# Performance work log

Hardware: AMD Instinct MI355X
Metric: run time of the kernel (lower is better)

The kernel has to match this reference:

```python
import jax, jax.numpy as jnp
import numpy as np

DN = ('NCHW', 'OIHW', 'NCHW')

def conv(x, w, b, stride=1, pad=1):
    y = jax.lax.conv_general_dilated(x, w, (stride, stride), [(pad, pad), (pad, pad)], dimension_numbers=DN)
    return y + b[None, :, None, None]

def conv_t(x, w, b):
    # torch ConvTranspose2d(k=4, s=2, p=1): implemented as lhs-dilated conv, pad = k-1-p = 2
    y = jax.lax.conv_general_dilated(x, w, (1, 1), [(2, 2), (2, 2)], lhs_dilation=(2, 2), dimension_numbers=DN)
    return y + b[None, :, None, None]

def residual_stack(x, rw3, rb3, rw1, rb1):
    # canonical VQ-VAE residual block: x + conv1x1(relu(conv3x3(relu(x)))), then final relu
    n = rw3.shape[0]
    for i in range(n):
        h = conv(jax.nn.relu(x), rw3[i], rb3[i], 1, 1)
        h = conv(jax.nn.relu(h), rw1[i], rb1[i], 1, 0)
        x = x + h
    return jax.nn.relu(x)

def vq(x, codebook, beta):
    # x: [N, D, H, W] -> [N, H, W, D]
    x = jnp.transpose(x, (0, 2, 3, 1))
    shp = x.shape
    xf = x.reshape(-1, shp[-1])                               # [T, D]
    d = (jnp.sum(xf * xf, 1, keepdims=True)
         + jnp.sum(codebook * codebook, 1)
         - 2.0 * xf @ codebook.T)                             # [T, K]
    idx = jnp.argmin(d, axis=1)                               # [T]
    enc = jax.nn.one_hot(idx, codebook.shape[0], dtype=x.dtype)
    q = jnp.take(codebook, idx, axis=0).reshape(shp)
    loss_e = jnp.mean((jax.lax.stop_gradient(q) - x) ** 2)
    loss_q = jnp.mean((q - jax.lax.stop_gradient(x)) ** 2)
    loss = loss_q + beta * loss_e
    q_st = x + jax.lax.stop_gradient(q - x)
    p = jnp.mean(enc, axis=0)
    perplexity = jnp.exp(-jnp.sum(p * jnp.log(p + 1e-10)))
    return loss, jnp.transpose(q_st, (0, 3, 1, 2)), perplexity, enc

def setup_inputs() -> dict:
    key = jax.random.key(0)
    ks = jax.random.split(key, 24)
    C_img, C, RH, NR, K, D = 3, 128, 32, 2, 512, 64
    def g(k, shape, fan_in):
        return jax.random.normal(k, shape, jnp.float32) * (1.0 / np.sqrt(fan_in))
    inp = {
        'x': jax.random.normal(ks[0], (16, C_img, 256, 256), jnp.float32),
        'enc_w1': g(ks[1], (C // 2, C_img, 4, 4), C_img * 16), 'enc_b1': jnp.zeros((C // 2,)),
        'enc_w2': g(ks[2], (C, C // 2, 4, 4), C // 2 * 16), 'enc_b2': jnp.zeros((C,)),
        'enc_w3': g(ks[3], (C, C, 3, 3), C * 9), 'enc_b3': jnp.zeros((C,)),
        'enc_rw3': g(ks[4], (NR, RH, C, 3, 3), C * 9), 'enc_rb3': jnp.zeros((NR, RH)),
        'enc_rw1': g(ks[5], (NR, C, RH, 1, 1), RH), 'enc_rb1': jnp.zeros((NR, C)),
        'pre_w': g(ks[6], (D, C, 1, 1), C), 'pre_b': jnp.zeros((D,)),
        'codebook': jax.random.uniform(ks[7], (K, D), jnp.float32, -1.0 / K, 1.0 / K),
        'dec_w1': g(ks[8], (C, D, 3, 3), D * 9), 'dec_b1': jnp.zeros((C,)),
        'dec_rw3': g(ks[9], (NR, RH, C, 3, 3), C * 9), 'dec_rb3': jnp.zeros((NR, RH)),
        'dec_rw1': g(ks[10], (NR, C, RH, 1, 1), RH), 'dec_rb1': jnp.zeros((NR, C)),
        'dec_dw1': g(ks[11], (C // 2, C, 4, 4), C * 16), 'dec_db1': jnp.zeros((C // 2,)),
        'dec_dw2': g(ks[12], (C_img, C // 2, 4, 4), C // 2 * 16), 'dec_db2': jnp.zeros((C_img,)),
    }
    return inp

def reference(x, enc_w1, enc_b1, enc_w2, enc_b2, enc_w3, enc_b3, enc_rw3, enc_rb3, enc_rw1, enc_rb1,
              pre_w, pre_b, codebook, dec_w1, dec_b1, dec_rw3, dec_rb3, dec_rw1, dec_rb1,
              dec_dw1, dec_db1, dec_dw2, dec_db2):
    beta = 0.25
    # encoder
    h = jax.nn.relu(conv(x, enc_w1, enc_b1, 2, 1))
    h = jax.nn.relu(conv(h, enc_w2, enc_b2, 2, 1))
    h = conv(h, enc_w3, enc_b3, 1, 1)
    h = residual_stack(h, enc_rw3, enc_rb3, enc_rw1, enc_rb1)
    # pre-VQ 1x1 conv
    z = conv(h, pre_w, pre_b, 1, 0)
    # vector quantization
    loss, q, perplexity, _ = vq(z, codebook, beta)
    # decoder
    d = conv(q, dec_w1, dec_b1, 1, 1)
    d = residual_stack(d, dec_rw3, dec_rb3, dec_rw1, dec_rb1)
    d = jax.nn.relu(conv_t(d, dec_dw1, dec_db1))
    x_recon = conv_t(d, dec_dw2, dec_db2)
    return loss, x_recon, perplexity
```

## Files before the change

kernel.cpp:

```cpp
#include <hip/hip_runtime.h>

typedef __attribute__((ext_vector_type(8)))  short bf16x8;
typedef __attribute__((ext_vector_type(16))) float f32x16;
typedef unsigned long long u64t;

__device__ __forceinline__ int swzu(int u)
{
    return u ^ (((u >> 3) & 1) | (((u >> 4) & 1) << 1));
}

__device__ __forceinline__ void fsplit(float v, unsigned short& h, unsigned short& l)
{
    union { float f; unsigned u; } a; a.f = v;
    unsigned uh = a.u + 0x7fffu + ((a.u >> 16) & 1u);
    h = (unsigned short)(uh >> 16);
    union { float f; unsigned u; } hb; hb.u = (unsigned)h << 16;
    float r = v - hb.f;
    union { float f; unsigned u; } b; b.f = r;
    unsigned ul = b.u + 0x7fffu + ((b.u >> 16) & 1u);
    l = (unsigned short)(ul >> 16);
}

__device__ __forceinline__ float bf2f(unsigned short u)
{
    union { float f; unsigned v; } a; a.v = (unsigned)u << 16; return a.f;
}

__global__ void pack_w(const float* __restrict__ w, unsigned short* __restrict__ hi,
                       unsigned short* __restrict__ lo, int Cout, int Cin, int KK,
                       int CoP, int CiP)
{
    int i = blockIdx.x * 256 + threadIdx.x;
    int tot = KK * CoP * CiP;
    if (i >= tot) return;
    int t  = i / (CoP * CiP);
    int r  = i - t * (CoP * CiP);
    int co = r / CiP;
    int ci = r - co * CiP;
    float v = (co < Cout && ci < Cin) ? w[((size_t)co * Cin + ci) * KK + t] : 0.f;
    unsigned short h, l;
    fsplit(v, h, l);
    hi[i] = h; lo[i] = l;
}

__global__ void cb_norm(const float* __restrict__ cb, float* __restrict__ cn)
{
    int i = blockIdx.x * 256 + threadIdx.x;
    if (i >= 512) return;
    float s = 0.f;
    for (int d = 0; d < 64; d++) s = fmaf(cb[i*64+d], cb[i*64+d], s);
    cn[i] = s;
}

__global__ __launch_bounds__(256) void pack_x(const float* __restrict__ x,
    unsigned short* __restrict__ PH)
{
    int idx = blockIdx.x * 256 + threadIdx.x;
    int n = idx >> 16, pix = idx & 65535;
    unsigned short h[8], l[8];
#pragma unroll
    for (int c = 0; c < 8; c++) h[c] = 0;
#pragma unroll
    for (int c = 0; c < 3; c++) {
        float v = x[((size_t)(n * 3 + c) << 16) + pix];
        fsplit(v, h[c], l[c]);
    }
    uint4 hv;
    hv.x = h[0] | ((unsigned)h[1] << 16); hv.y = h[2] | ((unsigned)h[3] << 16);
    hv.z = h[4] | ((unsigned)h[5] << 16); hv.w = h[6] | ((unsigned)h[7] << 16);
    uint4 z4 = make_uint4(0, 0, 0, 0);
    size_t b0 = (((size_t)(n * 2) << 16) + pix) * 8;
    size_t b1 = (((size_t)(n * 2 + 1) << 16) + pix) * 8;
    *(uint4*)(PH + b0) = hv;
    *(uint4*)(PH + b1) = z4;
}

template<int K,int S,int P,int CIP,int COUT,int HIN,int WIN,int HOUT,int WOUT,
         int TR,int TC,int WM,int WN,int PX2,int CO2,int CC,int CO_PAD,
         bool PACK,bool PRELU,bool PLO,bool WF32,bool ROUT,bool RES>
__global__ __launch_bounds__(256) void conv_mfma(
    const unsigned short* __restrict__ inH,
    const unsigned short* __restrict__ wpH,
    const float* __restrict__ bias, const float* __restrict__ res,
    float* __restrict__ outF, unsigned short* __restrict__ outPH,
    unsigned short* __restrict__ outPL)
{
    constexpr int IHT = (TR - 1) * S + K;
    constexpr int IW  = (TC - 1) * S + K;
    constexpr int PS  = IHT * IW;
    constexpr int PLN = CC * 2;
    constexpr int UN  = PS * PLN;
    constexpr int KK  = K * K;
    constexpr int NCH = CIP / (CC * 16);
    constexpr int CG  = CIP / 8;
    constexpr int CGO = (COUT + 7) / 8;
    constexpr int XB  = WOUT / TC;
    constexpr int REGU = (UN + 255) / 256;
    constexpr int NST = CC * KK;

    __shared__ uint4 lbH[UN];

    const int tid = threadIdx.x;
    const int bx  = blockIdx.x;
    const int r0  = (bx / XB) * TR;
    const int c0  = (bx % XB) * TC;
    const int co0 = blockIdx.y * (WM * CO2 * 32);
    const int n   = blockIdx.z;

    const int l  = tid & 63, wv = tid >> 6;
    const int wm = wv / WN, wn = wv % WN;
    const int ln = l & 31, kg = l >> 5;

    int pb[PX2], gyv[PX2], gxv[PX2];
#pragma unroll
    for (int p2 = 0; p2 < PX2; p2++) {
        int q = wn * (PX2 * 32) + p2 * 32 + ln;
        int lr = q / TC, lc = q % TC;
        pb[p2] = (lr * S) * IW + lc * S;
        gyv[p2] = r0 + lr; gxv[p2] = c0 + lc;
    }

    const int iy0 = r0 * S - P, ix0 = c0 * S - P;
    const size_t inb = (size_t)n * CG * HIN * WIN;

    f32x16 acc[PX2][CO2];
#pragma unroll
    for (int p2 = 0; p2 < PX2; p2++)
#pragma unroll
        for (int g = 0; g < CO2; g++) acc[p2][g] = (f32x16){};

    auto unit_load = [&](int u, int cgb, uint4& hv){
        int kgu = u / PS, pos = u - kgu * PS;
        int py = pos / IW, px = pos - py * IW;
        int gy = iy0 + py, gx = ix0 + px;
        bool ok = ((unsigned)gy < (unsigned)HIN) && ((unsigned)gx < (unsigned)WIN);
        hv = make_uint4(0,0,0,0);
        if (ok) {
            size_t a = (inb + ((size_t)(cgb + kgu) * HIN + gy) * WIN + gx) * 8;
            hv = *(const uint4*)(inH + a);
        }
    };

    auto stage_direct = [&](int kc){
        for (int idx = tid; idx < UN; idx += 256) {
            uint4 hv;
            unit_load(idx, kc * PLN, hv);
            lbH[swzu(idx)] = hv;
        }
    };

    uint4 rvH[REGU];
    auto load_regs = [&](int kc){
#pragma unroll
        for (int rr = 0; rr < REGU; rr++) {
            int idx = tid + rr * 256;
            uint4 hv = make_uint4(0,0,0,0);
            if (idx < UN) unit_load(idx, kc * PLN, hv);
            rvH[rr] = hv;
        }
    };
    auto write_regs = [&](){
#pragma unroll
        for (int rr = 0; rr < REGU; rr++) {
            int idx = tid + rr * 256;
            if (idx < UN) lbH[swzu(idx)] = rvH[rr];
        }
    };

    auto compute = [&](int kc){
        bf16x8 aC[CO2], aN[CO2], bC[PX2], bN[PX2];
        auto loadA = [&](int step, bf16x8* a){
            const int ks = step / KK, t = step - ks * KK;
#pragma unroll
            for (int g = 0; g < CO2; g++) {
                const int coA = co0 + (wm * CO2 + g) * 32 + ln;
                const size_t wo = ((size_t)t * CO_PAD + coA) * CIP
                                + kc * (CC * 16) + ks * 16 + kg * 8;
                a[g] = *(const bf16x8*)(wpH + wo);
            }
        };
        auto loadB = [&](int step, bf16x8* b){
            const int ks = step / KK, t = step - ks * KK;
            const int ky = t / K, kx = t - ky * K;
#pragma unroll
            for (int p2 = 0; p2 < PX2; p2++) {
                const int u = (ks * 2 + kg) * PS + pb[p2] + ky * IW + kx;
                b[p2] = *(const bf16x8*)&lbH[swzu(u)];
            }
        };
        loadA(0, aC); loadB(0, bC);
#pragma unroll
        for (int step = 0; step < NST; step++) {
            if (step + 1 < NST) { loadA(step + 1, aN); loadB(step + 1, bN); }
#pragma unroll
            for (int p2 = 0; p2 < PX2; p2++)
#pragma unroll
                for (int g = 0; g < CO2; g++)
                    acc[p2][g] = __builtin_amdgcn_mfma_f32_32x32x16_bf16(
                        aC[g], bC[p2], acc[p2][g], 0, 0, 0);
            if (step + 1 < NST) {
#pragma unroll
                for (int g = 0; g < CO2; g++) aC[g] = aN[g];
#pragma unroll
                for (int p2 = 0; p2 < PX2; p2++) bC[p2] = bN[p2];
            }
        }
    };

    stage_direct(0);
    __syncthreads();
    for (int kc = 0; kc < NCH; kc++) {
        const bool more = (kc + 1 < NCH);
        if (more) load_regs(kc + 1);
        compute(kc);
        if (more) {
            __syncthreads();
            write_regs();
            __syncthreads();
        }
    }

    const size_t HWo = (size_t)HOUT * WOUT;
#pragma unroll
    for (int p2 = 0; p2 < PX2; p2++) {
        const int gy = gyv[p2], gx = gxv[p2];
#pragma unroll
        for (int g = 0; g < CO2; g++) {
            const int co32 = co0 + (wm * CO2 + g) * 32;
#pragma unroll
            for (int rq = 0; rq < 4; rq++) {
                const int cb4 = co32 + 8 * rq + 4 * kg;
                float v[4];
#pragma unroll
                for (int i = 0; i < 4; i++) {
                    const int r = rq * 4 + i;
                    const int co = cb4 + i;
                    float bv = (co < COUT) ? bias[co] : 0.f;
                    float vv = acc[p2][g][r] + bv;
                    if (RES && co < COUT)
                        vv += res[((size_t)n * COUT + co) * HWo + (size_t)gy * WOUT + gx];
                    if (ROUT) vv = fmaxf(vv, 0.f);
                    if (WF32 && co < COUT)
                        outF[((size_t)n * COUT + co) * HWo + (size_t)gy * WOUT + gx] = vv;
                    v[i] = vv;
                }
                if (PACK) {
                    u64t uh = 0, ul = 0;
#pragma unroll
                    for (int i = 0; i < 4; i++) {
                        float pv = PRELU ? fmaxf(v[i], 0.f) : v[i];
                        unsigned short ph, pl;
                        fsplit(pv, ph, pl);
                        uh |= (u64t)ph << (16 * i);
                        ul |= (u64t)pl << (16 * i);
                    }
                    size_t pa = (((size_t)n * CGO + (co32 >> 3) + rq) * HOUT + gy) * (size_t)WOUT * 8
                              + (size_t)gx * 8 + 4 * kg;
                    *(u64t*)(outPH + pa) = uh;
                    if (PLO) *(u64t*)(outPL + pa) = ul;
                }
            }
        }
    }
}

template<int CIP,int COUT,int HW,int CO_PAD,
         bool PACK,bool PRELU,bool PLO,bool WF32,bool ROUT,bool RES>
__global__ __launch_bounds__(256) void conv1x1_mfma(
    const unsigned short* __restrict__ inH,
    const unsigned short* __restrict__ wpH,
    const float* __restrict__ bias, const float* __restrict__ res,
    float* __restrict__ outF, unsigned short* __restrict__ outPH,
    unsigned short* __restrict__ outPL)
{
    constexpr int NCH = CIP / 16;
    constexpr int CG  = CIP / 8;
    constexpr int CGO = (COUT + 7) / 8;

    const int tid = threadIdx.x;
    const int bx  = blockIdx.x;
    const int co0 = blockIdx.y * 64;
    const int n   = blockIdx.z;

    const int l  = tid & 63, wv = tid >> 6;
    const int wm = wv >> 1, wn = wv & 1;
    const int ln = l & 31, kg = l >> 5;

    const int pix = bx * 64 + wn * 32 + ln;
    const int coA = co0 + wm * 32 + ln;

    f32x16 acc = {};
#pragma unroll
    for (int kc = 0; kc < NCH; kc++) {
        bf16x8 b = *(const bf16x8*)(inH + ((size_t)(n * CG + kc * 2 + kg) * HW + pix) * 8);
        bf16x8 a = *(const bf16x8*)(wpH + ((size_t)coA * CIP + kc * 16 + kg * 8));
        acc = __builtin_amdgcn_mfma_f32_32x32x16_bf16(a, b, acc, 0, 0, 0);
    }

// ... 16 lines not shown
            v[i] = vv;
        }
        if (PACK) {
            u64t uh = 0, ul = 0;
#pragma unroll
            for (int i = 0; i < 4; i++) {
                float pv = PRELU ? fmaxf(v[i], 0.f) : v[i];
                unsigned short ph, pl;
                fsplit(pv, ph, pl);
                uh |= (u64t)ph << (16 * i);
                ul |= (u64t)pl << (16 * i);
            }
            size_t pa = (((size_t)n * CGO + (co32 >> 3) + rq) * HW + pix) * 8 + 4 * kg;
            *(u64t*)(outPH + pa) = uh;
            if (PLO) *(u64t*)(outPL + pa) = ul;
        }
    }
}

template<int CIP,int COUT,int HIN,int WIN,int CO2,int CC,int CO_PAD,
         bool PACK,bool WF32,bool ROUT>
__global__ __launch_bounds__(256) void convt_mfma(
    const unsigned short* __restrict__ inH,
    const unsigned short* __restrict__ wpH,
    const float* __restrict__ bias, float* __restrict__ outF,
    unsigned short* __restrict__ outPH)
{
    constexpr int HOUT = 2 * HIN, WOUT = 2 * WIN;
    constexpr int XHN  = WOUT / 128;
    constexpr int PS   = 3 * 68;
    constexpr int PLN  = CC * 2;
    constexpr int UN   = PS * PLN;
    constexpr int NCH  = CIP / (CC * 16);
    constexpr int CG   = CIP / 8;
    constexpr int CGO  = (COUT + 7) / 8;
    constexpr int REGU = (UN + 255) / 256;
    constexpr int NST  = CC * 4;

    __shared__ uint4 lbH[UN];

    const int tid = threadIdx.x;
    const int xh  = blockIdx.x % XHN;
    const int gr  = blockIdx.x / XHN;
    const int oy0 = (gr >> 1) * 4 + (gr & 1);
    const int co0 = blockIdx.y * (CO2 * 32);
    const int n   = blockIdx.z;

    const int ky0 = oy0 & 1;
    const int iyb = ((oy0 + ky0) >> 1) - 1;

    const int l  = tid & 63, wv = tid >> 6;
    const int pw = wv & 1, xb = wv >> 1;
    const int ln = l & 31, kg = l >> 5;

    const size_t inb = (size_t)n * CG * HIN * WIN;

    f32x16 acc[2][CO2];
#pragma unroll
    for (int r2 = 0; r2 < 2; r2++)
#pragma unroll
        for (int g = 0; g < CO2; g++) acc[r2][g] = (f32x16){};

    auto unit_load = [&](int u, int cgb, uint4& hv){
        int kgu = u / PS, pos = u - kgu * PS;
        int rr = pos / 68, cc = pos - rr * 68;
        int gy = iyb + rr, gx = xh * 64 + cc - 1;
        bool ok = ((unsigned)gy < (unsigned)HIN) && ((unsigned)gx < (unsigned)WIN);
        hv = make_uint4(0,0,0,0);
        if (ok) {
            size_t a = (inb + ((size_t)(cgb + kgu) * HIN + gy) * WIN + gx) * 8;
            hv = *(const uint4*)(inH + a);
        }
    };

    auto stage_direct = [&](int kc){
        for (int idx = tid; idx < UN; idx += 256) {
            uint4 hv;
            unit_load(idx, kc * PLN, hv);
            lbH[swzu(idx)] = hv;
        }
    };

    uint4 rvH[REGU];
    auto load_regs = [&](int kc){
#pragma unroll
        for (int rr = 0; rr < REGU; rr++) {
            int idx = tid + rr * 256;
            uint4 hv = make_uint4(0,0,0,0);
            if (idx < UN) unit_load(idx, kc * PLN, hv);
            rvH[rr] = hv;
        }
    };
    auto write_regs = [&](){
#pragma unroll
        for (int rr = 0; rr < REGU; rr++) {
            int idx = tid + rr * 256;
            if (idx < UN) lbH[swzu(idx)] = rvH[rr];
        }
    };

    auto compute = [&](int kc){
        bf16x8 aC[CO2], aN[CO2], bC[2], bN[2];
        auto loadA = [&](int step, bf16x8* a){
            const int ks = step / 4, tt = step - ks * 4;
            const int widx = (ky0 + 2 * (tt >> 1)) * 4 + (pw + 2 * (tt & 1));
#pragma unroll
            for (int g = 0; g < CO2; g++) {
                const int coA = co0 + g * 32 + ln;
                const size_t wo = ((size_t)widx * CO_PAD + coA) * CIP
                                + kc * (CC * 16) + ks * 16 + kg * 8;
                a[g] = *(const bf16x8*)(wpH + wo);
            }
        };
        auto loadB = [&](int step, bf16x8* b){
            const int ks = step / 4, tt = step - ks * 4;
            const int ty = tt >> 1, tx = tt & 1;
#pragma unroll
            for (int r2 = 0; r2 < 2; r2++) {
                const int u = (ks * 2 + kg) * PS + (r2 + ty) * 68 + xb * 32 + ln + pw + tx;
                b[r2] = *(const bf16x8*)&lbH[swzu(u)];
            }
        };
        loadA(0, aC); loadB(0, bC);
#pragma unroll
        for (int step = 0; step < NST; step++) {
            if (step + 1 < NST) { loadA(step + 1, aN); loadB(step + 1, bN); }
#pragma unroll
            for (int r2 = 0; r2 < 2; r2++)
#pragma unroll
                for (int g = 0; g < CO2; g++)
                    acc[r2][g] = __builtin_amdgcn_mfma_f32_32x32x16_bf16(
                        aC[g], bC[r2], acc[r2][g], 0, 0, 0);
            if (step + 1 < NST) {
#pragma unroll
                for (int g = 0; g < CO2; g++) aC[g] = aN[g];
#pragma unroll
                for (int r2 = 0; r2 < 2; r2++) bC[r2] = bN[r2];
            }
        }
    };

    stage_direct(0);
    __syncthreads();
    for (int kc = 0; kc < NCH; kc++) {
        const bool more = (kc + 1 < NCH);
        if (more) load_regs(kc + 1);
        compute(kc);
        if (more) {
            __syncthreads();
            write_regs();
            __syncthreads();
        }
    }

    const int ox = xh * 128 + pw + 2 * (xb * 32 + ln);
    const size_t HWo = (size_t)HOUT * WOUT;
#pragma unroll
    for (int r2 = 0; r2 < 2; r2++) {
        const int oy = oy0 + 2 * r2;
#pragma unroll
        for (int g = 0; g < CO2; g++) {
            const int co32 = co0 + g * 32;
#pragma unroll
            for (int rq = 0; rq < 4; rq++) {
                const int cb4 = co32 + 8 * rq + 4 * kg;
                float v[4];
#pragma unroll
                for (int i = 0; i < 4; i++) {
                    const int r = rq * 4 + i;
                    const int co = cb4 + i;
                    float bv = (co < COUT) ? bias[co] : 0.f;
                    float vv = acc[r2][g][r] + bv;
                    if (ROUT) vv = fmaxf(vv, 0.f);
                    if (WF32 && co < COUT)
                        outF[((size_t)n * COUT + co) * HWo + (size_t)oy * WOUT + ox] = vv;
                    v[i] = vv;
                }
                if (PACK) {
                    u64t uh = 0;
#pragma unroll
                    for (int i = 0; i < 4; i++) {
                        unsigned short ph, pl;
                        fsplit(v[i], ph, pl);
                        uh |= (u64t)ph << (16 * i);
// ... 68 lines not shown
        for (int r = 0; r < 16; r++) {
            int m    = (r & 3) + 8 * (r >> 2) + 4 * kg;
            int code = cg * 32 + m;
            float s  = a0[r] + a1[r];
            float dm = cnl[code] - 2.f * s;
            if (dm < bm) { bm = dm; bidx = code; }
        }
    }

    float bm2 = __shfl_xor(bm, 32);
    int   bi2 = __shfl_xor(bidx, 32);
    if (bm2 < bm || (bm2 == bm && bi2 < bidx)) { bm = bm2; bidx = bi2; }

    {
        int t = blk * 128 + tok;
        int n = t >> 12, pix = t & 4095;
#pragma unroll
        for (int cgl = 0; cgl < 4; cgl++) {
            int cg = kg * 4 + cgl;
            uint4 hv = *(const uint4*)(cbH + (size_t)bidx * 64 + cg * 8);
            size_t a = (((size_t)(n * 8 + cg)) * 4096 + pix) * 8;
            *(uint4*)(qPH + a) = hv;
        }
    }

    float bestd = xn + bm;
    float c = (kg == 0) ? bestd : 0.f;
#pragma unroll
    for (int o = 32; o > 0; o >>= 1) c += __shfl_down(c, o, 64);
    if (l == 0) ssep[blk * 4 + wv] = c;
    if (kg == 0) atomicAdd(&hl[bidx], 1);
    __syncthreads();
    for (int i = tid; i < 512; i += 256) if (hl[i] > 0) atomicAdd(&hist[i], hl[i]);
}

__global__ void vq_init(int* hist)
{
    for (int i = threadIdx.x; i < 512; i += 256) hist[i] = 0;
}

__global__ __launch_bounds__(256) void vq_finalize(
    const float* __restrict__ ssep, const int* __restrict__ hist,
    float* __restrict__ o_loss, float* __restrict__ o_perp)
{
    __shared__ float red[256];
    const int tid = threadIdx.x;
    float h = 0.f;
    for (int i = tid; i < 512; i += 256) {
        float p = (float)hist[i] * (1.0f / 65536.0f);
        h -= p * logf(p + 1e-10f);
    }
    red[tid] = h;
    __syncthreads();
    for (int st = 128; st > 0; st >>= 1) {
        if (tid < st) red[tid] += red[tid + st];
        __syncthreads();
    }
    const float H = red[0];
    __syncthreads();
    float s = 0.f;
    for (int i = tid; i < 2048; i += 256) s += ssep[i];
    red[tid] = s;
    __syncthreads();
    for (int st = 128; st > 0; st >>= 1) {
        if (tid < st) red[tid] += red[tid + st];
        __syncthreads();
    }
    if (tid == 0) {
        *o_loss = 1.25f * red[0] / 4194304.0f;
        *o_perp = expf(H);
    }
// ... 14 lines not shown
    const float* enc_rb3 = (const float*)d_in[8];
    const float* enc_rw1 = (const float*)d_in[9];
    const float* enc_rb1 = (const float*)d_in[10];
    const float* pre_w   = (const float*)d_in[11];
    const float* pre_b   = (const float*)d_in[12];
    const float* cb      = (const float*)d_in[13];
    const float* dec_w1  = (const float*)d_in[14];
    const float* dec_b1  = (const float*)d_in[15];
    const float* dec_rw3 = (const float*)d_in[16];
    const float* dec_rb3 = (const float*)d_in[17];
    const float* dec_rw1 = (const float*)d_in[18];
    const float* dec_rb1 = (const float*)d_in[19];
    const float* dw1     = (const float*)d_in[20];
    const float* db1     = (const float*)d_in[21];
    const float* dw2     = (const float*)d_in[22];
    const float* db2     = (const float*)d_in[23];

    float* o      = (float*)d_out;
    float* loss_p = o;
    float* recon  = o + 1;
    float* perp_p = o + 1 + 16 * 3 * 256 * 256;

    unsigned short* R1H = (unsigned short*)d_ws;
    unsigned short* R1L = R1H + 16777216;
    unsigned short* R2H = R1L + 16777216;
    unsigned short* R2L = R2H + 16777216;
    float* Cf  = (float*)(R2L + 16777216);
    float* SSE = Cf + 8388608;
    int*   HIST = (int*)(SSE + 2048);

    unsigned short *xPH = R1H;
    unsigned short *BPH = R1H;
    unsigned short *zPH = R1H + 8388608, *zPL = R1L + 8388608;
    unsigned short *DtPH = R1H + 12582912;
    unsigned short *dAPH = R1H;
    unsigned short *APH = R2H;
    unsigned short *CPH = R2H;
    unsigned short *qPH = R2H + 8388608;

    unsigned short* wp_cur = (unsigned short*)(((size_t)(HIST + 512) + 31) & ~(size_t)31);
    auto carve = [&](size_t n_us) {
        unsigned short* p = wp_cur;
        wp_cur += ((n_us + 15) & ~(size_t)15);
        return p;
    };
    auto PK = [&](const float* w, unsigned short* hi, unsigned short* lo,
                  int Co, int Ci, int KK, int CoP, int CiP) {
        int tot = KK * CoP * CiP;
        pack_w<<<dim3((tot + 255) / 256), dim3(256), 0, stream>>>(w, hi, lo, Co, Ci, KK, CoP, CiP);
    };

    unsigned short *e1H = carve(16*64*16),  *e1L = carve(16*64*16);
    unsigned short *e2H = carve(16*128*64), *e2L = carve(16*128*64);
    unsigned short *e3H = carve(9*128*128), *e3L = carve(9*128*128);
    unsigned short *er3aH = carve(9*32*128), *er3aL = carve(9*32*128);
    unsigned short *er3bH = carve(9*32*128), *er3bL = carve(9*32*128);
    unsigned short *er1aH = carve(128*32),   *er1aL = carve(128*32);
    unsigned short *er1bH = carve(128*32),   *er1bL = carve(128*32);
    unsigned short *preH = carve(64*128),    *preL = carve(64*128);
    unsigned short *d1H  = carve(9*128*64),  *d1L  = carve(9*128*64);
    unsigned short *dr3aH = carve(9*32*128), *dr3aL = carve(9*32*128);
    unsigned short *dr3bH = carve(9*32*128), *dr3bL = carve(9*32*128);
    unsigned short *dr1aH = carve(128*32),   *dr1aL = carve(128*32);
    unsigned short *dr1bH = carve(128*32),   *dr1bL = carve(128*32);
    unsigned short *ct1H = carve(16*64*128), *ct1L = carve(16*64*128);
    unsigned short *ct2H = carve(16*32*64),  *ct2L = carve(16*32*64);
    unsigned short *cbH  = carve(512*64),    *cbL  = carve(512*64);
    float* CN = (float*)carve(1024);

    PK(enc_w1, e1H, e1L, 64, 3, 16, 64, 16);
    PK(enc_w2, e2H, e2L, 128, 64, 16, 128, 64);
    PK(enc_w3, e3H, e3L, 128, 128, 9, 128, 128);
    PK(enc_rw3,             er3aH, er3aL, 32, 128, 9, 32, 128);
    PK(enc_rw3 + 32*128*9,  er3bH, er3bL, 32, 128, 9, 32, 128);
    PK(enc_rw1,             er1aH, er1aL, 128, 32, 1, 128, 32);
    PK(enc_rw1 + 128*32,    er1bH, er1bL, 128, 32, 1, 128, 32);
    PK(pre_w, preH, preL, 64, 128, 1, 64, 128);
    PK(dec_w1, d1H, d1L, 128, 64, 9, 128, 64);
    PK(dec_rw3,             dr3aH, dr3aL, 32, 128, 9, 32, 128);
    PK(dec_rw3 + 32*128*9,  dr3bH, dr3bL, 32, 128, 9, 32, 128);
    PK(dec_rw1,             dr1aH, dr1aL, 128, 32, 1, 128, 32);
    PK(dec_rw1 + 128*32,    dr1bH, dr1bL, 128, 32, 1, 128, 32);
    PK(dw1, ct1H, ct1L, 64, 128, 16, 64, 128);
    PK(dw2, ct2H, ct2L, 3, 64, 16, 32, 64);
    PK(cb,  cbH,  cbL,  512, 64, 1, 512, 64);
    cb_norm<<<dim3(2), dim3(256), 0, stream>>>(cb, CN);
    pack_x<<<dim3(4096), dim3(256), 0, stream>>>(x, xPH);

    const int N = 16;

    conv_mfma<4,2,1, 16,64, 256,256, 128,128, 2,64, 2,2,2,1, 1, 64,
              true,false,false,false,true,false>
        <<<dim3(128,1,N),256,0,stream>>>(xPH, e1H, enc_b1, nullptr, nullptr, APH, nullptr);
    conv_mfma<4,2,1, 64,128, 128,128, 64,64, 2,64, 2,2,2,2, 1, 128,
              true,false,false,false,true,false>
        <<<dim3(32,1,N),256,0,stream>>>(APH, e2H, enc_b2, nullptr, nullptr, BPH, nullptr);
    conv_mfma<3,1,1, 128,128, 64,64, 64,64, 2,64, 2,2,2,2, 2, 128,
              true,true,false,true,false,false>
        <<<dim3(32,1,N),256,0,stream>>>(BPH, e3H, enc_b3, nullptr, Cf, CPH, nullptr);
    conv_mfma<3,1,1, 128,32, 64,64, 64,64, 4,64, 1,4,2,1, 2, 32,
              true,true,false,false,false,false>
        <<<dim3(16,1,N),256,0,stream>>>(CPH, er3aH, enc_rb3, nullptr, nullptr, DtPH, nullptr);
    conv1x1_mfma<32,128, 4096, 128,  true,true,false,true,false,true>
        <<<dim3(64,2,N),256,0,stream>>>(DtPH, er1aH, enc_rb1, Cf, Cf, CPH, nullptr);
    conv_mfma<3,1,1, 128,32, 64,64, 64,64, 4,64, 1,4,2,1, 2, 32,
              true,true,false,false,false,false>
        <<<dim3(16,1,N),256,0,stream>>>(CPH, er3bH, enc_rb3 + 32, nullptr, nullptr, DtPH, nullptr);
    conv1x1_mfma<32,128, 4096, 128,  true,true,false,true,false,true>
        <<<dim3(64,2,N),256,0,stream>>>(DtPH, er1bH, enc_rb1 + 128, Cf, Cf, CPH, nullptr);
    conv1x1_mfma<128,64, 4096, 64,   true,false,true,false,false,false>
        <<<dim3(64,1,N),256,0,stream>>>(CPH, preH, pre_b, nullptr, nullptr, zPH, zPL);

    vq_init<<<dim3(1), dim3(256), 0, stream>>>(HIST);
    vq_mfma<<<dim3(512), dim3(256), 0, stream>>>(zPH, zPL, cbH, cbL, CN, qPH, SSE, HIST);
    vq_finalize<<<dim3(1), dim3(256), 0, stream>>>(SSE, HIST, loss_p, perp_p);

    conv_mfma<3,1,1, 64,128, 64,64, 64,64, 2,64, 2,2,2,2, 2, 128,
              true,true,false,true,false,false>
        <<<dim3(32,1,N),256,0,stream>>>(qPH, d1H, dec_b1, nullptr, Cf, CPH, nullptr);
    conv_mfma<3,1,1, 128,32, 64,64, 64,64, 4,64, 1,4,2,1, 2, 32,
              true,true,false,false,false,false>
        <<<dim3(16,1,N),256,0,stream>>>(CPH, dr3aH, dec_rb3, nullptr, nullptr, DtPH, nullptr);
    conv1x1_mfma<32,128, 4096, 128,  true,true,false,true,false,true>
        <<<dim3(64,2,N),256,0,stream>>>(DtPH, dr1aH, dec_rb1, Cf, Cf, CPH, nullptr);
    conv_mfma<3,1,1, 128,32, 64,64, 64,64, 4,64, 1,4,2,1, 2, 32,
              true,true,false,false,false,false>
        <<<dim3(16,1,N),256,0,stream>>>(CPH, dr3bH, dec_rb3 + 32, nullptr, nullptr, DtPH, nullptr);
    conv1x1_mfma<32,128, 4096, 128,  true,true,false,true,false,true>
        <<<dim3(64,2,N),256,0,stream>>>(DtPH, dr1bH, dec_rb1 + 128, Cf, Cf, CPH, nullptr);
    convt_mfma<128,64, 64,64, 2, 2, 64,  true,false,true>
        <<<dim3(64,1,N),256,0,stream>>>(CPH, ct1H, db1, nullptr, dAPH);
    convt_mfma<64,3, 128,128, 1, 2, 32,  false,true,false>
        <<<dim3(256,1,N),256,0,stream>>>(dAPH, ct2H, db2, recon, nullptr);
}
```

Before: 520.9 us.

## Double-buffer LDS staging, deepen weight prefetch, and retile conv launches

The conv and transposed-conv kernels now keep two LDS input buffers. The next channel chunk is written into the idle buffer, so each chunk boundary needs one barrier instead of two. Weight fragments are prefetched two steps ahead through a three-slot register ring, and LDS B fragments one step ahead through a two-slot ring, replacing the register copy shuffles. Separately, the encoder and decoder conv launches use smaller row tiles with different warp layouts, giving twice as many blocks to improve occupancy, at the cost of more halo reloads and doubled LDS use per block.

```diff
diff --git a/kernel.cpp b/kernel.cpp
--- a/kernel.cpp
+++ b/kernel.cpp
@@ -92,13 +92,14 @@
     constexpr int UN  = PS * PLN;
     constexpr int KK  = K * K;
     constexpr int NCH = CIP / (CC * 16);
+    constexpr int NBUF = (NCH > 1) ? 2 : 1;
     constexpr int CG  = CIP / 8;
     constexpr int CGO = (COUT + 7) / 8;
     constexpr int XB  = WOUT / TC;
     constexpr int REGU = (UN + 255) / 256;
     constexpr int NST = CC * KK;
 
-    __shared__ uint4 lbH[UN];
+    __shared__ uint4 lbH[NBUF * UN];
 
     const int tid = threadIdx.x;
     const int bx  = blockIdx.x;
@@ -141,11 +142,11 @@
         }
     };
 
-    auto stage_direct = [&](int kc){
+    auto stage_direct = [&](int kc, int b){
         for (int idx = tid; idx < UN; idx += 256) {
             uint4 hv;
             unit_load(idx, kc * PLN, hv);
-            lbH[swzu(idx)] = hv;
+            lbH[b * UN + swzu(idx)] = hv;
         }
     };
 
@@ -159,17 +160,17 @@
             rvH[rr] = hv;
         }
     };
-    auto write_regs = [&](){
+    auto write_regs = [&](int b){
 #pragma unroll
         for (int rr = 0; rr < REGU; rr++) {
             int idx = tid + rr * 256;
-            if (idx < UN) lbH[swzu(idx)] = rvH[rr];
-        }
-    };
-
-    auto compute = [&](int kc){
-        bf16x8 aC[CO2], aN[CO2], bC[PX2], bN[PX2];
-        auto loadA = [&](int step, bf16x8* a){
+            if (idx < UN) lbH[b * UN + swzu(idx)] = rvH[rr];
+        }
+    };
+
+    auto compute = [&](int kc, int b){
+        bf16x8 aR[3][CO2], bR[2][PX2];
+        auto loadA = [&](int step, bf16x8 (&a)[CO2]){
             const int ks = step / KK, t = step - ks * KK;
 #pragma unroll
             for (int g = 0; g < CO2; g++) {
@@ -179,44 +180,42 @@
                 a[g] = *(const bf16x8*)(wpH + wo);
             }
         };
-        auto loadB = [&](int step, bf16x8* b){
+        auto loadB = [&](int step, bf16x8 (&bv)[PX2]){
             const int ks = step / KK, t = step - ks * KK;
             const int ky = t / K, kx = t - ky * K;
 #pragma unroll
             for (int p2 = 0; p2 < PX2; p2++) {
                 const int u = (ks * 2 + kg) * PS + pb[p2] + ky * IW + kx;
-                b[p2] = *(const bf16x8*)&lbH[swzu(u)];
+                bv[p2] = *(const bf16x8*)&lbH[b * UN + swzu(u)];
             }
         };
-        loadA(0, aC); loadB(0, bC);
+        loadA(0, aR[0]);
+        if (NST > 1) loadA(1, aR[1]);
+        loadB(0, bR[0]);
 #pragma unroll
         for (int step = 0; step < NST; step++) {
-            if (step + 1 < NST) { loadA(step + 1, aN); loadB(step + 1, bN); }
+            if (step + 2 < NST) loadA(step + 2, aR[(step + 2) % 3]);
+            if (step + 1 < NST) loadB(step + 1, bR[(step + 1) & 1]);
 #pragma unroll
             for (int p2 = 0; p2 < PX2; p2++)
 #pragma unroll
                 for (int g = 0; g < CO2; g++)
                     acc[p2][g] = __builtin_amdgcn_mfma_f32_32x32x16_bf16(
-                        aC[g], bC[p2], acc[p2][g], 0, 0, 0);
-            if (step + 1 < NST) {
-#pragma unroll
-                for (int g = 0; g < CO2; g++) aC[g] = aN[g];
-#pragma unroll
-                for (int p2 = 0; p2 < PX2; p2++) bC[p2] = bN[p2];
-            }
-        }
-    };
-
-    stage_direct(0);
+                        aR[step % 3][g], bR[step & 1][p2], acc[p2][g], 0, 0, 0);
+        }
+    };
+
+    stage_direct(0, 0);
     __syncthreads();
+    int cur = 0;
     for (int kc = 0; kc < NCH; kc++) {
         const bool more = (kc + 1 < NCH);
         if (more) load_regs(kc + 1);
-        compute(kc);
+        compute(kc, cur);
         if (more) {
+            write_regs(cur ^ 1);
             __syncthreads();
-            write_regs();
-            __syncthreads();
+            cur ^= 1;
         }
     }
 
@@ -346,12 +345,13 @@
     constexpr int PLN  = CC * 2;
     constexpr int UN   = PS * PLN;
     constexpr int NCH  = CIP / (CC * 16);
+    constexpr int NBUF = (NCH > 1) ? 2 : 1;
     constexpr int CG   = CIP / 8;
     constexpr int CGO  = (COUT + 7) / 8;
     constexpr int REGU = (UN + 255) / 256;
     constexpr int NST  = CC * 4;
 
-    __shared__ uint4 lbH[UN];
+    __shared__ uint4 lbH[NBUF * UN];
 
     const int tid = threadIdx.x;
     const int xh  = blockIdx.x % XHN;
@@ -387,11 +387,11 @@
         }
     };
 
-    auto stage_direct = [&](int kc){
+    auto stage_direct = [&](int kc, int b){
         for (int idx = tid; idx < UN; idx += 256) {
             uint4 hv;
             unit_load(idx, kc * PLN, hv);
-            lbH[swzu(idx)] = hv;
+            lbH[b * UN + swzu(idx)] = hv;
         }
     };
 
@@ -405,17 +405,17 @@
             rvH[rr] = hv;
         }
     };
-    auto write_regs = [&](){
+    auto write_regs = [&](int b){
 #pragma unroll
         for (int rr = 0; rr < REGU; rr++) {
             int idx = tid + rr * 256;
-            if (idx < UN) lbH[swzu(idx)] = rvH[rr];
-        }
-    };
-
-    auto compute = [&](int kc){
-        bf16x8 aC[CO2], aN[CO2], bC[2], bN[2];
-        auto loadA = [&](int step, bf16x8* a){
+            if (idx < UN) lbH[b * UN + swzu(idx)] = rvH[rr];
+        }
+    };
+
+    auto compute = [&](int kc, int b){
+        bf16x8 aR[3][CO2], bR[2][2];
+        auto loadA = [&](int step, bf16x8 (&a)[CO2]){
             const int ks = step / 4, tt = step - ks * 4;
             const int widx = (ky0 + 2 * (tt >> 1)) * 4 + (pw + 2 * (tt & 1));
 #pragma unroll
@@ -426,44 +426,42 @@
                 a[g] = *(const bf16x8*)(wpH + wo);
             }
         };
-        auto loadB = [&](int step, bf16x8* b){
+        auto loadB = [&](int step, bf16x8 (&bv)[2]){
             const int ks = step / 4, tt = step - ks * 4;
             const int ty = tt >> 1, tx = tt & 1;
 #pragma unroll
             for (int r2 = 0; r2 < 2; r2++) {
                 const int u = (ks * 2 + kg) * PS + (r2 + ty) * 68 + xb * 32 + ln + pw + tx;
-                b[r2] = *(const bf16x8*)&lbH[swzu(u)];
+                bv[r2] = *(const bf16x8*)&lbH[b * UN + swzu(u)];
             }
         };
-        loadA(0, aC); loadB(0, bC);
+        loadA(0, aR[0]);
+        if (NST > 1) loadA(1, aR[1]);
+        loadB(0, bR[0]);
 #pragma unroll
         for (int step = 0; step < NST; step++) {
-            if (step + 1 < NST) { loadA(step + 1, aN); loadB(step + 1, bN); }
+            if (step + 2 < NST) loadA(step + 2, aR[(step + 2) % 3]);
+            if (step + 1 < NST) loadB(step + 1, bR[(step + 1) & 1]);
 #pragma unroll
             for (int r2 = 0; r2 < 2; r2++)
 #pragma unroll
                 for (int g = 0; g < CO2; g++)
                     acc[r2][g] = __builtin_amdgcn_mfma_f32_32x32x16_bf16(
-                        aC[g], bC[r2], acc[r2][g], 0, 0, 0);
-            if (step + 1 < NST) {
-#pragma unroll
-                for (int g = 0; g < CO2; g++) aC[g] = aN[g];
-#pragma unroll
-                for (int r2 = 0; r2 < 2; r2++) bC[r2] = bN[r2];
-            }
-        }
-    };
-
-    stage_direct(0);
+                        aR[step % 3][g], bR[step & 1][r2], acc[r2][g], 0, 0, 0);
+        }
+    };
+
+    stage_direct(0, 0);
     __syncthreads();
+    int cur = 0;
     for (int kc = 0; kc < NCH; kc++) {
         const bool more = (kc + 1 < NCH);
         if (more) load_regs(kc + 1);
-        compute(kc);
+        compute(kc, cur);
         if (more) {
+            write_regs(cur ^ 1);
             __syncthreads();
-            write_regs();
-            __syncthreads();
+            cur ^= 1;
         }
     }
 
@@ -740,23 +738,23 @@
 
     const int N = 16;
 
-    conv_mfma<4,2,1, 16,64, 256,256, 128,128, 2,64, 2,2,2,1, 1, 64,
+    conv_mfma<4,2,1, 16,64, 256,256, 128,128, 1,64, 2,2,1,1, 1, 64,
               true,false,false,false,true,false>
-        <<<dim3(128,1,N),256,0,stream>>>(xPH, e1H, enc_b1, nullptr, nullptr, APH, nullptr);
-    conv_mfma<4,2,1, 64,128, 128,128, 64,64, 2,64, 2,2,2,2, 1, 128,
+        <<<dim3(256,1,N),256,0,stream>>>(xPH, e1H, enc_b1, nullptr, nullptr, APH, nullptr);
+    conv_mfma<4,2,1, 64,128, 128,128, 64,64, 1,64, 4,1,2,1, 1, 128,
               true,false,false,false,true,false>
-        <<<dim3(32,1,N),256,0,stream>>>(APH, e2H, enc_b2, nullptr, nullptr, BPH, nullptr);
-    conv_mfma<3,1,1, 128,128, 64,64, 64,64, 2,64, 2,2,2,2, 2, 128,
+        <<<dim3(64,1,N),256,0,stream>>>(APH, e2H, enc_b2, nullptr, nullptr, BPH, nullptr);
+    conv_mfma<3,1,1, 128,128, 64,64, 64,64, 1,64, 4,1,2,1, 2, 128,
               true,true,false,true,false,false>
-        <<<dim3(32,1,N),256,0,stream>>>(BPH, e3H, enc_b3, nullptr, Cf, CPH, nullptr);
-    conv_mfma<3,1,1, 128,32, 64,64, 64,64, 4,64, 1,4,2,1, 2, 32,
+        <<<dim3(64,1,N),256,0,stream>>>(BPH, e3H, enc_b3, nullptr, Cf, CPH, nullptr);
+    conv_mfma<3,1,1, 128,32, 64,64, 64,64, 2,64, 1,4,1,1, 4, 32,
               true,true,false,false,false,false>
-        <<<dim3(16,1,N),256,0,stream>>>(CPH, er3aH, enc_rb3, nullptr, nullptr, DtPH, nullptr);
+        <<<dim3(32,1,N),256,0,stream>>>(CPH, er3aH, enc_rb3, nullptr, nullptr, DtPH, nullptr);
     conv1x1_mfma<32,128, 4096, 128,  true,true,false,true,false,true>
         <<<dim3(64,2,N),256,0,stream>>>(DtPH, er1aH, enc_rb1, Cf, Cf, CPH, nullptr);
-    conv_mfma<3,1,1, 128,32, 64,64, 64,64, 4,64, 1,4,2,1, 2, 32,
+    conv_mfma<3,1,1, 128,32, 64,64, 64,64, 2,64, 1,4,1,1, 4, 32,
               true,true,false,false,false,false>
-        <<<dim3(16,1,N),256,0,stream>>>(CPH, er3bH, enc_rb3 + 32, nullptr, nullptr, DtPH, nullptr);
+        <<<dim3(32,1,N),256,0,stream>>>(CPH, er3bH, enc_rb3 + 32, nullptr, nullptr, DtPH, nullptr);
     conv1x1_mfma<32,128, 4096, 128,  true,true,false,true,false,true>
         <<<dim3(64,2,N),256,0,stream>>>(DtPH, er1bH, enc_rb1 + 128, Cf, Cf, CPH, nullptr);
     conv1x1_mfma<128,64, 4096, 64,   true,false,true,false,false,false>
@@ -766,17 +764,17 @@
     vq_mfma<<<dim3(512), dim3(256), 0, stream>>>(zPH, zPL, cbH, cbL, CN, qPH, SSE, HIST);
     vq_finalize<<<dim3(1), dim3(256), 0, stream>>>(SSE, HIST, loss_p, perp_p);
 
-    conv_mfma<3,1,1, 64,128, 64,64, 64,64, 2,64, 2,2,2,2, 2, 128,
+    conv_mfma<3,1,1, 64,128, 64,64, 64,64, 1,64, 4,1,2,1, 2, 128,
               true,true,false,true,false,false>
-        <<<dim3(32,1,N),256,0,stream>>>(qPH, d1H, dec_b1, nullptr, Cf, CPH, nullptr);
-    conv_mfma<3,1,1, 128,32, 64,64, 64,64, 4,64, 1,4,2,1, 2, 32,
+        <<<dim3(64,1,N),256,0,stream>>>(qPH, d1H, dec_b1, nullptr, Cf, CPH, nullptr);
+    conv_mfma<3,1,1, 128,32, 64,64, 64,64, 2,64, 1,4,1,1, 4, 32,
               true,true,false,false,false,false>
-        <<<dim3(16,1,N),256,0,stream>>>(CPH, dr3aH, dec_rb3, nullptr, nullptr, DtPH, nullptr);
+        <<<dim3(32,1,N),256,0,stream>>>(CPH, dr3aH, dec_rb3, nullptr, nullptr, DtPH, nullptr);
     conv1x1_mfma<32,128, 4096, 128,  true,true,false,true,false,true>
         <<<dim3(64,2,N),256,0,stream>>>(DtPH, dr1aH, dec_rb1, Cf, Cf, CPH, nullptr);
-    conv_mfma<3,1,1, 128,32, 64,64, 64,64, 4,64, 1,4,2,1, 2, 32,
+    conv_mfma<3,1,1, 128,32, 64,64, 64,64, 2,64, 1,4,1,1, 4, 32,
               true,true,false,false,false,false>
-        <<<dim3(16,1,N),256,0,stream>>>(CPH, dr3bH, dec_rb3 + 32, nullptr, nullptr, DtPH, nullptr);
+        <<<dim3(32,1,N),256,0,stream>>>(CPH, dr3bH, dec_rb3 + 32, nullptr, nullptr, DtPH, nullptr);
     conv1x1_mfma<32,128, 4096, 128,  true,true,false,true,false,true>
         <<<dim3(64,2,N),256,0,stream>>>(DtPH, dr1bH, dec_rb1 + 128, Cf, Cf, CPH, nullptr);
     convt_mfma<128,64, 64,64, 2, 2, 64,  true,false,true>
```

Result: slower. 552.7 us (+6.1%).

## Fuse residual 3x3 and 1x1 convs into one kernel, batch weight packing

Applied to the files above, without the earlier changes.

Adds a fused_res kernel that computes the residual block's 3x3 conv (128->32), keeps the ReLU'd 32-channel intermediate in shared memory, then applies the 1x1 conv (32->128) with bias, residual add and output packing. This removes the intermediate global write/read and halves the residual-stage launches, and ping-pongs between two packed buffers so a block's input isn't overwritten by its own output. It also merges the sixteen weight-packing launches into one descriptor-driven kernel and folds the histogram init into the codebook-norm kernel. The fused kernel uses one MFMA accumulator per wave for the 3x3 stage, so occupancy and MFMA utilisation may differ from the separate kernels.

```diff
diff --git a/kernel.cpp b/kernel.cpp
--- a/kernel.cpp
+++ b/kernel.cpp
@@ -26,30 +26,45 @@
     union { float f; unsigned v; } a; a.v = (unsigned)u << 16; return a.f;
 }
 
-__global__ void pack_w(const float* __restrict__ w, unsigned short* __restrict__ hi,
-                       unsigned short* __restrict__ lo, int Cout, int Cin, int KK,
-                       int CoP, int CiP)
-{
-    int i = blockIdx.x * 256 + threadIdx.x;
-    int tot = KK * CoP * CiP;
+struct PackDesc {
+    const float* w;
+    unsigned short *hi, *lo;
+    int Co, Ci, KK, CoP, CiP;
+    int blk0;
+};
+struct PackAll { PackDesc d[16]; int nd; };
+
+__global__ __launch_bounds__(256) void pack_all(PackAll pa)
+{
+    int bx = blockIdx.x;
+    int di = 0;
+#pragma unroll
+    for (int i = 0; i < 16; i++)
+        if (i < pa.nd && bx >= pa.d[i].blk0) di = i;
+    const PackDesc& D = pa.d[di];
+    int i = (bx - D.blk0) * 256 + threadIdx.x;
+    int tot = D.KK * D.CoP * D.CiP;
     if (i >= tot) return;
-    int t  = i / (CoP * CiP);
-    int r  = i - t * (CoP * CiP);
-    int co = r / CiP;
-    int ci = r - co * CiP;
-    float v = (co < Cout && ci < Cin) ? w[((size_t)co * Cin + ci) * KK + t] : 0.f;
+    int t  = i / (D.CoP * D.CiP);
+    int r  = i - t * (D.CoP * D.CiP);
+    int co = r / D.CiP;
+    int ci = r - co * D.CiP;
+    float v = (co < D.Co && ci < D.Ci) ? D.w[((size_t)co * D.Ci + ci) * D.KK + t] : 0.f;
     unsigned short h, l;
     fsplit(v, h, l);
-    hi[i] = h; lo[i] = l;
-}
-
-__global__ void cb_norm(const float* __restrict__ cb, float* __restrict__ cn)
+    D.hi[i] = h; D.lo[i] = l;
+}
+
+__global__ __launch_bounds__(256) void vq_prep(const float* __restrict__ cb,
+                                               float* __restrict__ cn, int* __restrict__ hist)
 {
     int i = blockIdx.x * 256 + threadIdx.x;
-    if (i >= 512) return;
-    float s = 0.f;
-    for (int d = 0; d < 64; d++) s = fmaf(cb[i*64+d], cb[i*64+d], s);
-    cn[i] = s;
+    if (i < 512) {
+        hist[i] = 0;
+        float s = 0.f;
+        for (int d = 0; d < 64; d++) s = fmaf(cb[i*64+d], cb[i*64+d], s);
+        cn[i] = s;
+    }
 }
 
 __global__ __launch_bounds__(256) void pack_x(const float* __restrict__ x,
@@ -264,6 +279,167 @@
     }
 }
 
+__global__ __launch_bounds__(256) void fused_res(
+    const unsigned short* __restrict__ inH,
+    const unsigned short* __restrict__ w3H,
+    const float* __restrict__ b3,
+    const unsigned short* __restrict__ w1H,
+    const float* __restrict__ b1,
+    float* __restrict__ Cf,
+    unsigned short* __restrict__ outPH)
+{
+    constexpr int H = 64, W = 64;
+    constexpr int IHT = 4, IW = 66, PS = IHT * IW;
+    constexpr int CC = 2, PLN = 4, UN = PS * PLN;
+    constexpr int NCH = 4, NST = 18;
+    constexpr int REGU = (UN + 255) / 256;
+    constexpr int CG = 16, CGO = 16;
+
+    __shared__ uint4 lbH[UN];
+    __shared__ unsigned short midL[4 * 128 * 8];
+
+    const int tid = threadIdx.x;
+    const int r0  = blockIdx.x * 2;
+    const int n   = blockIdx.z;
+    const int l  = tid & 63, wv = tid >> 6;
+    const int ln = l & 31, kg = l >> 5;
+
+    const int pxl1 = wv * 32 + ln;
+    const int lr1 = pxl1 / W, lc1 = pxl1 % W;
+    const int pb1 = lr1 * IW + lc1;
+
+    const int iy0 = r0 - 1, ix0 = -1;
+    const size_t inb = (size_t)n * CG * H * W;
+
+    auto unit_load = [&](int u, int cgb, uint4& hv){
+        int kgu = u / PS, pos = u - kgu * PS;
+        int py = pos / IW, px = pos - py * IW;
+        int gy = iy0 + py, gx = ix0 + px;
+        bool ok = ((unsigned)gy < (unsigned)H) && ((unsigned)gx < (unsigned)W);
+        hv = make_uint4(0,0,0,0);
+        if (ok) {
+            size_t a = (inb + ((size_t)(cgb + kgu) * H + gy) * W + gx) * 8;
+            hv = *(const uint4*)(inH + a);
+        }
+    };
+    auto stage_direct = [&](int kc){
+        for (int idx = tid; idx < UN; idx += 256) {
+            uint4 hv;
+            unit_load(idx, kc * PLN, hv);
+            lbH[swzu(idx)] = hv;
+        }
+    };
+    uint4 rvH[REGU];
+    auto load_regs = [&](int kc){
+#pragma unroll
+        for (int rr = 0; rr < REGU; rr++) {
+            int idx = tid + rr * 256;
+            uint4 hv = make_uint4(0,0,0,0);
+            if (idx < UN) unit_load(idx, kc * PLN, hv);
+            rvH[rr] = hv;
+        }
+    };
+    auto write_regs = [&](){
+#pragma unroll
+        for (int rr = 0; rr < REGU; rr++) {
+            int idx = tid + rr * 256;
+            if (idx < UN) lbH[swzu(idx)] = rvH[rr];
+        }
+    };
+
+    f32x16 acc1 = {};
+    auto compute = [&](int kc){
+        bf16x8 aC, aN, bC, bN;
+        auto loadA = [&](int step, bf16x8& a){
+            const int ks = step / 9, t = step - ks * 9;
+            a = *(const bf16x8*)(w3H + ((size_t)t * 32 + ln) * 128
+                                 + kc * 32 + ks * 16 + kg * 8);
+        };
+        auto loadB = [&](int step, bf16x8& b){
+            const int ks = step / 9, t = step - ks * 9;
+            const int ky = t / 3, kx = t - ky * 3;
+            const int u = (ks * 2 + kg) * PS + pb1 + ky * IW + kx;
+            b = *(const bf16x8*)&lbH[swzu(u)];
+        };
+        loadA(0, aC); loadB(0, bC);
+#pragma unroll
+        for (int step = 0; step < NST; step++) {
+            if (step + 1 < NST) { loadA(step + 1, aN); loadB(step + 1, bN); }
+            acc1 = __builtin_amdgcn_mfma_f32_32x32x16_bf16(aC, bC, acc1, 0, 0, 0);
+            if (step + 1 < NST) { aC = aN; bC = bN; }
+        }
+    };
+
+    stage_direct(0);
+    __syncthreads();
+    for (int kc = 0; kc < NCH; kc++) {
+        const bool more = (kc + 1 < NCH);
+        if (more) load_regs(kc + 1);
+        compute(kc);
+        if (more) {
+            __syncthreads();
+            write_regs();
+            __syncthreads();
+        }
+    }
+
+#pragma unroll
+    for (int r = 0; r < 16; r++) {
+        const int co = (r & 3) + 8 * (r >> 2) + 4 * kg;
+        float vv = fmaxf(acc1[r] + b3[co], 0.f);
+        unsigned short h, lo_;
+        fsplit(vv, h, lo_);
+        midL[((co >> 3) * 128 + pxl1) * 8 + (co & 7)] = h;
+    }
+    __syncthreads();
+
+    f32x16 acc2[4];
+#pragma unroll
+    for (int pg = 0; pg < 4; pg++) acc2[pg] = (f32x16){};
+#pragma unroll
+    for (int pg = 0; pg < 4; pg++) {
+#pragma unroll
+        for (int ks = 0; ks < 2; ks++) {
+            bf16x8 b = *(const bf16x8*)&midL[((ks * 2 + kg) * 128 + pg * 32 + ln) * 8];
+            bf16x8 a = *(const bf16x8*)(w1H + ((size_t)(wv * 32 + ln)) * 32
+                                        + ks * 16 + kg * 8);
+            acc2[pg] = __builtin_amdgcn_mfma_f32_32x32x16_bf16(a, b, acc2[pg], 0, 0, 0);
+        }
+    }
+
+    const int co32 = wv * 32;
+#pragma unroll
+    for (int pg = 0; pg < 4; pg++) {
+        const int pxl = pg * 32 + ln;
+        const int gy = r0 + pxl / W, gx = pxl % W;
+#pragma unroll
+        for (int rq = 0; rq < 4; rq++) {
+            const int cb4 = co32 + 8 * rq + 4 * kg;
+            float v[4];
+#pragma unroll
+            for (int i = 0; i < 4; i++) {
+                const int r = rq * 4 + i;
+                const int co = cb4 + i;
+                size_t ra = ((size_t)n * 128 + co) * (H * W) + (size_t)gy * W + gx;
+                float vv = acc2[pg][r] + b1[co] + Cf[ra];
+                Cf[ra] = vv;
+                v[i] = vv;
+            }
+            u64t uh = 0;
+#pragma unroll
+            for (int i = 0; i < 4; i++) {
+                float pv = fmaxf(v[i], 0.f);
+                unsigned short ph, pl;
+                fsplit(pv, ph, pl);
+                uh |= (u64t)ph << (16 * i);
+            }
+            size_t pa = (((size_t)n * CGO + (co32 >> 3) + rq) * H + gy) * (size_t)W * 8
+                      + (size_t)gx * 8 + 4 * kg;
+            *(u64t*)(outPH + pa) = uh;
+        }
+    }
+}
+
 template<int CIP,int COUT,int HW,int CO_PAD,
          bool PACK,bool PRELU,bool PLO,bool WF32,bool ROUT,bool RES>
 __global__ __launch_bounds__(256) void conv1x1_mfma(
@@ -426,13 +602,13 @@
                 a[g] = *(const bf16x8*)(wpH + wo);
             }
         };
-        auto loadB = [&](int step, bf16x8* b){
+        auto loadB = [&](int step, bf16x8* bv){
             const int ks = step / 4, tt = step - ks * 4;
             const int ty = tt >> 1, tx = tt & 1;
 #pragma unroll
             for (int r2 = 0; r2 < 2; r2++) {
                 const int u = (ks * 2 + kg) * PS + (r2 + ty) * 68 + xb * 32 + ln + pw + tx;
-                b[r2] = *(const bf16x8*)&lbH[swzu(u)];
+                bv[r2] = *(const bf16x8*)&lbH[swzu(u)];
             }
         };
         loadA(0, aC); loadB(0, bC);
@@ -598,11 +774,6 @@
     if (kg == 0) atomicAdd(&hl[bidx], 1);
     __syncthreads();
     for (int i = tid; i < 512; i += 256) if (hl[i] > 0) atomicAdd(&hist[i], hl[i]);
-}
-
-__global__ void vq_init(int* hist)
-{
-    for (int i = threadIdx.x; i < 512; i += 256) hist[i] = 0;
 }
 
 __global__ __launch_bounds__(256) void vq_finalize(
@@ -683,10 +854,10 @@
     unsigned short *xPH = R1H;
     unsigned short *BPH = R1H;
     unsigned short *zPH = R1H + 8388608, *zPL = R1L + 8388608;
-    unsigned short *DtPH = R1H + 12582912;
     unsigned short *dAPH = R1H;
     unsigned short *APH = R2H;
-    unsigned short *CPH = R2H;
+    unsigned short *C1PH = R2H;
+    unsigned short *C2PH = R2L;
     unsigned short *qPH = R2H + 8388608;
 
     unsigned short* wp_cur = (unsigned short*)(((size_t)(HIST + 512) + 31) & ~(size_t)31);
@@ -694,11 +865,6 @@
         unsigned short* p = wp_cur;
         wp_cur += ((n_us + 15) & ~(size_t)15);
         return p;
-    };
-    auto PK = [&](const float* w, unsigned short* hi, unsigned short* lo,
-                  int Co, int Ci, int KK, int CoP, int CiP) {
-        int tot = KK * CoP * CiP;
-        pack_w<<<dim3((tot + 255) / 256), dim3(256), 0, stream>>>(w, hi, lo, Co, Ci, KK, CoP, CiP);
     };
 
     unsigned short *e1H = carve(16*64*16),  *e1L = carve(16*64*16);
@@ -719,23 +885,31 @@
     unsigned short *cbH  = carve(512*64),    *cbL  = carve(512*64);
     float* CN = (float*)carve(1024);
 
-    PK(enc_w1, e1H, e1L, 64, 3, 16, 64, 16);
-    PK(enc_w2, e2H, e2L, 128, 64, 16, 128, 64);
-    PK(enc_w3, e3H, e3L, 128, 128, 9, 128, 128);
-    PK(enc_rw3,             er3aH, er3aL, 32, 128, 9, 32, 128);
-    PK(enc_rw3 + 32*128*9,  er3bH, er3bL, 32, 128, 9, 32, 128);
-    PK(enc_rw1,             er1aH, er1aL, 128, 32, 1, 128, 32);
-    PK(enc_rw1 + 128*32,    er1bH, er1bL, 128, 32, 1, 128, 32);
-    PK(pre_w, preH, preL, 64, 128, 1, 64, 128);
-    PK(dec_w1, d1H, d1L, 128, 64, 9, 128, 64);
-    PK(dec_rw3,             dr3aH, dr3aL, 32, 128, 9, 32, 128);
-    PK(dec_rw3 + 32*128*9,  dr3bH, dr3bL, 32, 128, 9, 32, 128);
-    PK(dec_rw1,             dr1aH, dr1aL, 128, 32, 1, 128, 32);
-    PK(dec_rw1 + 128*32,    dr1bH, dr1bL, 128, 32, 1, 128, 32);
-    PK(dw1, ct1H, ct1L, 64, 128, 16, 64, 128);
-    PK(dw2, ct2H, ct2L, 3, 64, 16, 32, 64);
-    PK(cb,  cbH,  cbL,  512, 64, 1, 512, 64);
-    cb_norm<<<dim3(2), dim3(256), 0, stream>>>(cb, CN);
+    PackAll pa; int nb = 0;
+    auto addPK = [&](int i, const float* w, unsigned short* hi, unsigned short* lo,
+                     int Co, int Ci, int KK, int CoP, int CiP) {
+        pa.d[i] = {w, hi, lo, Co, Ci, KK, CoP, CiP, nb};
+        nb += (KK * CoP * CiP + 255) / 256;
+    };
+    addPK(0,  enc_w1, e1H, e1L, 64, 3, 16, 64, 16);
+    addPK(1,  enc_w2, e2H, e2L, 128, 64, 16, 128, 64);
+    addPK(2,  enc_w3, e3H, e3L, 128, 128, 9, 128, 128);
+    addPK(3,  enc_rw3,            er3aH, er3aL, 32, 128, 9, 32, 128);
+    addPK(4,  enc_rw3 + 32*128*9, er3bH, er3bL, 32, 128, 9, 32, 128);
+    addPK(5,  enc_rw1,            er1aH, er1aL, 128, 32, 1, 128, 32);
+    addPK(6,  enc_rw1 + 128*32,   er1bH, er1bL, 128, 32, 1, 128, 32);
+    addPK(7,  pre_w, preH, preL, 64, 128, 1, 64, 128);
+    addPK(8,  dec_w1, d1H, d1L, 128, 64, 9, 128, 64);
+    addPK(9,  dec_rw3,            dr3aH, dr3aL, 32, 128, 9, 32, 128);
+    addPK(10, dec_rw3 + 32*128*9, dr3bH, dr3bL, 32, 128, 9, 32, 128);
+    addPK(11, dec_rw1,            dr1aH, dr1aL, 128, 32, 1, 128, 32);
+    addPK(12, dec_rw1 + 128*32,   dr1bH, dr1bL, 128, 32, 1, 128, 32);
+    addPK(13, dw1, ct1H, ct1L, 64, 128, 16, 64, 128);
+    addPK(14, dw2, ct2H, ct2L, 3, 64, 16, 32, 64);
+    addPK(15, cb,  cbH,  cbL,  512, 64, 1, 512, 64);
+    pa.nd = 16;
+    pack_all<<<dim3(nb), dim3(256), 0, stream>>>(pa);
+    vq_prep<<<dim3(2), dim3(256), 0, stream>>>(cb, CN, HIST);
     pack_x<<<dim3(4096), dim3(256), 0, stream>>>(x, xPH);
 
     const int N = 16;
@@ -748,39 +922,22 @@
         <<<dim3(32,1,N),256,0,stream>>>(APH, e2H, enc_b2, nullptr, nullptr, BPH, nullptr);
     conv_mfma<3,1,1, 128,128, 64,64, 64,64, 2,64, 2,2,2,2, 2, 128,
               true,true,false,true,false,false>
-        <<<dim3(32,1,N),256,0,stream>>>(BPH, e3H, enc_b3, nullptr, Cf, CPH, nullptr);
-    conv_mfma<3,1,1, 128,32, 64,64, 64,64, 4,64, 1,4,2,1, 2, 32,
-              true,true,false,false,false,false>
-        <<<dim3(16,1,N),256,0,stream>>>(CPH, er3aH, enc_rb3, nullptr, nullptr, DtPH, nullptr);
-    conv1x1_mfma<32,128, 4096, 128,  true,true,false,true,false,true>
-        <<<dim3(64,2,N),256,0,stream>>>(DtPH, er1aH, enc_rb1, Cf, Cf, CPH, nullptr);
-    conv_mfma<3,1,1, 128,32, 64,64, 64,64, 4,64, 1,4,2,1, 2, 32,
-              true,true,false,false,false,false>
-        <<<dim3(16,1,N),256,0,stream>>>(CPH, er3bH, enc_rb3 + 32, nullptr, nullptr, DtPH, nullptr);
-    conv1x1_mfma<32,128, 4096, 128,  true,true,false,true,false,true>
-        <<<dim3(64,2,N),256,0,stream>>>(DtPH, er1bH, enc_rb1 + 128, Cf, Cf, CPH, nullptr);
+        <<<dim3(32,1,N),256,0,stream>>>(BPH, e3H, enc_b3, nullptr, Cf, C1PH, nullptr);
+    fused_res<<<dim3(32,1,N),256,0,stream>>>(C1PH, er3aH, enc_rb3, er1aH, enc_rb1, Cf, C2PH);
+    fused_res<<<dim3(32,1,N),256,0,stream>>>(C2PH, er3bH, enc_rb3 + 32, er1bH, enc_rb1 + 128, Cf, C1PH);
     conv1x1_mfma<128,64, 4096, 64,   true,false,true,false,false,false>
-        <<<dim3(64,1,N),256,0,stream>>>(CPH, preH, pre_b, nullptr, nullptr, zPH, zPL);
-
-    vq_init<<<dim3(1), dim3(256), 0, stream>>>(HIST);
+        <<<dim3(64,1,N),256,0,stream>>>(C1PH, preH, pre_b, nullptr, nullptr, zPH, zPL);
+
     vq_mfma<<<dim3(512), dim3(256), 0, stream>>>(zPH, zPL, cbH, cbL, CN, qPH, SSE, HIST);
     vq_finalize<<<dim3(1), dim3(256), 0, stream>>>(SSE, HIST, loss_p, perp_p);
 
     conv_mfma<3,1,1, 64,128, 64,64, 64,64, 2,64, 2,2,2,2, 2, 128,
               true,true,false,true,false,false>
-        <<<dim3(32,1,N),256,0,stream>>>(qPH, d1H, dec_b1, nullptr, Cf, CPH, nullptr);
-    conv_mfma<3,1,1, 128,32, 64,64, 64,64, 4,64, 1,4,2,1, 2, 32,
-              true,true,false,false,false,false>
-        <<<dim3(16,1,N),256,0,stream>>>(CPH, dr3aH, dec_rb3, nullptr, nullptr, DtPH, nullptr);
-    conv1x1_mfma<32,128, 4096, 128,  true,true,false,true,false,true>
-        <<<dim3(64,2,N),256,0,stream>>>(DtPH, dr1aH, dec_rb1, Cf, Cf, CPH, nullptr);
-    conv_mfma<3,1,1, 128,32, 64,64, 64,64, 4,64, 1,4,2,1, 2, 32,
-              true,true,false,false,false,false>
-        <<<dim3(16,1,N),256,0,stream>>>(CPH, dr3bH, dec_rb3 + 32, nullptr, nullptr, DtPH, nullptr);
-    conv1x1_mfma<32,128, 4096, 128,  true,true,false,true,false,true>
-        <<<dim3(64,2,N),256,0,stream>>>(DtPH, dr1bH, dec_rb1 + 128, Cf, Cf, CPH, nullptr);
+        <<<dim3(32,1,N),256,0,stream>>>(qPH, d1H, dec_b1, nullptr, Cf, C1PH, nullptr);
+    fused_res<<<dim3(32,1,N),256,0,stream>>>(C1PH, dr3aH, dec_rb3, dr1aH, dec_rb1, Cf, C2PH);
+    fused_res<<<dim3(32,1,N),256,0,stream>>>(C2PH, dr3bH, dec_rb3 + 32, dr1bH, dec_rb1 + 128, Cf, C1PH);
     convt_mfma<128,64, 64,64, 2, 2, 64,  true,false,true>
-        <<<dim3(64,1,N),256,0,stream>>>(CPH, ct1H, db1, nullptr, dAPH);
+        <<<dim3(64,1,N),256,0,stream>>>(C1PH, ct1H, db1, nullptr, dAPH);
     convt_mfma<64,3, 128,128, 1, 2, 32,  false,true,false>
         <<<dim3(256,1,N),256,0,stream>>>(dAPH, ct2H, db2, recon, nullptr);
 }
```

Measured after the change: 462.3 us. 11.3% less time.
